# Optimization experiments

Measured on AMD Instinct MI355X. Metric: run time of the kernel, lower is better.

Reference implementation:

```python
import jax, jax.numpy as jnp
import numpy as np

B, OBS, H, A, E = 131072, 194, 64, 5, 3  # batch, obs dim, hidden, max_action_dim, n event types


def setup_inputs() -> dict:
    key = jax.random.key(0)
    ks = jax.random.split(key, 16)
    s = lambda k, shape, std=0.1: (jax.random.normal(k, shape, dtype=jnp.float32) * std)
    return {
        "x": jax.random.normal(ks[0], (B, OBS), dtype=jnp.float32),
        "action": jax.random.randint(ks[1], (B,), 0, A),
        "W1": s(ks[2], (OBS, H)), "b1": jnp.zeros((H,), jnp.float32),
        "W2": s(ks[3], (H, H)),   "b2": jnp.zeros((H,), jnp.float32),
        "Wh": s(ks[4], (E, H, A), 0.01), "bh": jnp.zeros((E, A), jnp.float32),
        "Wc1": s(ks[5], (OBS, H)), "bc1": jnp.zeros((H,), jnp.float32),
        "Wc2": s(ks[6], (H, H)),   "bc2": jnp.zeros((H,), jnp.float32),
        "Wc3": s(ks[7], (H, 1)),   "bc3": jnp.zeros((1,), jnp.float32),
    }


def reference(x, action, W1, b1, W2, b2, Wh, bh, Wc1, bc1, Wc2, bc2, Wc3, bc3):
    # shared trunk
    feat = jnp.tanh(jnp.tanh(x @ W1 + b1) @ W2 + b2)          # [B, H]
    # route each sample to one of E heads via argmax of first 3 obs dims
    ev = jnp.argmax(x[:, :E], axis=1)                          # [B] int
    all_logits = jnp.einsum('bh,eha->bea', feat, Wh) + bh      # [B, E, A]
    logits = jnp.take_along_axis(
        all_logits, jnp.broadcast_to(ev[:, None, None], (x.shape[0], 1, A)), axis=1
    )[:, 0]                                                    # [B, A]
    logp_all = jax.nn.log_softmax(logits, axis=-1)             # [B, A]
    logp = jnp.take_along_axis(logp_all, action[:, None], axis=1)[:, 0]  # [B]
    entropy = -jnp.sum(jnp.exp(logp_all) * logp_all, axis=-1)  # [B]
    # critic
    value = jnp.tanh(jnp.tanh(x @ Wc1 + bc1) @ Wc2 + bc2) @ Wc3 + bc3    # [B, 1]
    return action, logp, entropy, value
```

## Files before the change

kernel.cpp:

```cpp
#include <hip/hip_runtime.h>
#include <hip/hip_bf16.h>

constexpr int Bt    = 131072;
constexpr int OBS   = 194;

constexpr int W1B_S  = 0;
constexpr int WC1B_S = 14336;
constexpr int W2B_S  = 28672;
constexpr int WC2B_S = 36864;
constexpr int WHB_S  = 45056;
constexpr size_t EVG_B = 98304;
constexpr size_t HG_S  = 131072;

typedef short bf8   __attribute__((ext_vector_type(8)));
typedef float f32x4 __attribute__((ext_vector_type(4)));
typedef unsigned int u32;

__device__ __forceinline__ short f2bs(float f) {
    union { __hip_bfloat16 h; short s; } u;
    u.h = __float2bfloat16(f);
    return u.s;
}
__device__ __forceinline__ float bs2f(short s) {
    union { short s; __hip_bfloat16 h; } u;
    u.s = s;
    return __bfloat162float(u.h);
}
__device__ __forceinline__ u32 pk2(float a, float b) {
    union { __hip_bfloat162 h; u32 u; } r;
    r.h = __float22bfloat162_rn(float2{a, b});
    return r.u;
}
__device__ __forceinline__ float fast_tanh(float v) {
    v = fminf(fmaxf(v, -15.f), 15.f);
    float e = __expf(2.f * v);
    return (e - 1.f) * __builtin_amdgcn_rcpf(e + 1.f);
}
__device__ __forceinline__ void dma16(const void* g, void* s) {
    __builtin_amdgcn_global_load_lds(
        (const __attribute__((address_space(1))) u32*)g,
        (__attribute__((address_space(3))) u32*)s, 16, 0, 0);
}

__global__ void __launch_bounds__(256) prep(
    const float* __restrict__ W1, const float* __restrict__ b1,
    const float* __restrict__ W2, const float* __restrict__ Wh,
    const float* __restrict__ Wc1, const float* __restrict__ bc1,
    const float* __restrict__ Wc2, const float* __restrict__ Wc3,
    short* __restrict__ ws)
{
    const int gid = blockIdx.x * 256 + threadIdx.x;
    const int gsz = gridDim.x * 256;

    for (int i = gid; i < 14336; i += gsz) {
        int j = i & 7, l = (i >> 3) & 63, nt = (i >> 9) & 3, kb = i >> 11;
        int k = kb * 32 + ((l >> 4) << 3) + j;
        int n = nt * 16 + (l & 15);
        short v1 = 0, v2 = 0;
        if (k < OBS) {
            v1 = f2bs(W1[k * 64 + n]);
            v2 = f2bs(Wc1[k * 64 + n]);
        } else if (k == OBS) {
            v1 = f2bs(b1[n]);
            v2 = f2bs(bc1[n]);
        }
        ws[W1B_S + i]  = v1;
        ws[WC1B_S + i] = v2;
    }
    for (int i = gid; i < 8192; i += gsz) {
        int j = i & 7, l = (i >> 3) & 63, nt = (i >> 9) & 3, kb = i >> 11;
        int s = kb * 32 + ((l >> 4) << 3) + j;
        int kp = (s & 3) * 16 + (s >> 2);
        int n = nt * 16 + (l & 15);
        ws[W2B_S + i]  = f2bs(W2[kp * 64 + n]);
        ws[WC2B_S + i] = f2bs(Wc2[kp * 64 + n]);
    }
    for (int i = gid; i < 1024; i += gsz) {
        int j = i & 7, l = (i >> 3) & 63, kb = i >> 9;
        int s = kb * 32 + ((l >> 4) << 3) + j;
        int kp = (s & 3) * 16 + (s >> 2);
        int cc = l & 15;
        float v;
        if (cc == 15) v = Wc3[kp];
        else { int e = cc / 5, a = cc - 5 * e; v = Wh[(e * 64 + kp) * 5 + a]; }
        ws[WHB_S + i] = f2bs(v);
    }
}

__global__ void __launch_bounds__(512, 2) trunk1(
    const float* __restrict__ x, const short* __restrict__ ws,
    short* __restrict__ hG, unsigned char* __restrict__ evG)
{
    __shared__ __align__(16) char smem[57344];
    const int t = threadIdx.x;
    const int l = t & 63, q = (t >> 4) & 3, c = t & 15;
    const int wu = __builtin_amdgcn_readfirstlane(t >> 6);

    #pragma unroll
    for (int i = 0; i < 7; ++i) {
        int ch = wu * 7 + i;
        dma16((const char*)ws + ch * 1024 + l * 16, smem + ch * 1024);
    }

    const bf8* fW1L  = reinterpret_cast<const bf8*>(smem);
    const bf8* fWc1L = reinterpret_cast<const bf8*>(smem + 28672);

    const int tt = blockIdx.x * 8 + wu;
    const float* xr = x + (size_t)tt * 16 * OBS + (size_t)c * OBS;

    union AF { u32 u[4]; bf8 v; } af[7];
    float4 f40;
    #pragma unroll
    for (int kb = 0; kb < 6; ++kb) {
        float4 a = *reinterpret_cast<const float4*>(xr + kb * 32 + q * 8);
        float4 b = *reinterpret_cast<const float4*>(xr + kb * 32 + q * 8 + 4);
        if (kb == 0) f40 = a;
        af[kb].u[0] = pk2(a.x, a.y);
        af[kb].u[1] = pk2(a.z, a.w);
        af[kb].u[2] = pk2(b.x, b.y);
        af[kb].u[3] = pk2(b.z, b.w);
    }
    af[6].u[0] = 0; af[6].u[1] = 0; af[6].u[2] = 0; af[6].u[3] = 0;
    if (q == 0) {
        float2 v = *reinterpret_cast<const float2*>(xr + 192);
        af[6].u[0] = pk2(v.x, v.y);
        af[6].u[1] = pk2(1.0f, 0.0f);
    }
    if (l < 16) {
        int ev = 0; float b = f40.x;
        if (f40.y > b) { b = f40.y; ev = 1; }
        if (f40.z > b) ev = 2;
        evG[tt * 16 + l] = (unsigned char)ev;
    }

    __syncthreads();

    f32x4 aa[4], ac[4];
    #pragma unroll
    for (int nt = 0; nt < 4; ++nt) {
        aa[nt] = f32x4{0.f, 0.f, 0.f, 0.f};
        ac[nt] = f32x4{0.f, 0.f, 0.f, 0.f};
    }
    #pragma unroll
    for (int kb = 0; kb < 7; ++kb) {
        bf8 a = af[kb].v;
        #pragma unroll
        for (int nt = 0; nt < 4; ++nt) {
            aa[nt] = __builtin_amdgcn_mfma_f32_16x16x32_bf16(a, fW1L [(kb * 4 + nt) * 64 + l], aa[nt], 0, 0, 0);
            ac[nt] = __builtin_amdgcn_mfma_f32_16x16x32_bf16(a, fWc1L[(kb * 4 + nt) * 64 + l], ac[nt], 0, 0, 0);
        }
    }

    short* hGt = hG + (size_t)tt * 2048;
    #pragma unroll
    for (int r = 0; r < 4; ++r) {
        uint2 pa, pc;
        pa.x = pk2(fast_tanh(aa[0][r]), fast_tanh(aa[1][r]));
        pa.y = pk2(fast_tanh(aa[2][r]), fast_tanh(aa[3][r]));
        pc.x = pk2(fast_tanh(ac[0][r]), fast_tanh(ac[1][r]));
        pc.y = pk2(fast_tanh(ac[2][r]), fast_tanh(ac[3][r]));
        *reinterpret_cast<uint2*>(hGt + (r * 4 + q) * 64 + 4 * c)        = pa;
        *reinterpret_cast<uint2*>(hGt + 1024 + (r * 4 + q) * 64 + 4 * c) = pc;
    }
}

constexpr int F2_W   = 34816;
constexpr int F2_PW  = 5248;
constexpr int F2_LDS = F2_W + 8 * F2_PW;

__global__ void __launch_bounds__(512, 2) head2(
    const int* __restrict__ act_in,
    const float* __restrict__ b2, const float* __restrict__ bc2,
    const float* __restrict__ bh, const float* __restrict__ bc3,
    const short* __restrict__ ws,
    const short* __restrict__ hG, const unsigned char* __restrict__ evG,
    float* __restrict__ out)
{
    __shared__ __align__(16) char smem[F2_LDS];
    const int t = threadIdx.x;
    const int l = t & 63, q = (t >> 4) & 3, c = t & 15;
    const int wu = __builtin_amdgcn_readfirstlane(t >> 6);

    #pragma unroll
    for (int i = 0; i < 5; ++i) {
        int ch = wu + i * 8;
        if (ch < 34)
            dma16((const char*)ws + 57344 + ch * 1024 + l * 16, smem + ch * 1024);
    }

    float b2v[4], bc2v[4];
    #pragma unroll
    for (int nt = 0; nt < 4; ++nt) {
        b2v[nt]  = b2[nt * 16 + c];
        bc2v[nt] = bc2[nt * 16 + c];
    }
    float bhv = (c < 15) ? bh[c] : bc3[0];

    __syncthreads();

    const bf8* fW2L  = reinterpret_cast<const bf8*>(smem);
    const bf8* fWc2L = reinterpret_cast<const bf8*>(smem + 16384);
    const bf8* fWhL  = reinterpret_cast<const bf8*>(smem + 32768);
    short* ha = reinterpret_cast<short*>(smem + F2_W + wu * F2_PW);
    short* hc = ha + 1152;
    short* lw = reinterpret_cast<short*>(smem + F2_W + wu * F2_PW + 4608);
    float* vb = reinterpret_cast<float*>(smem + F2_W + wu * F2_PW + 5184);

    #pragma unroll 1
    for (int i = 0; i < 2; ++i) {
        const int tt = blockIdx.x * 16 + wu * 2 + i;
        const int gm = tt * 16 + c;
        int act = 0, evc = 0;
        if (l < 16) { act = act_in[gm]; evc = evG[gm]; }

        const short* hGt = hG + (size_t)tt * 2048;
        uint2 va[4], vc2[4];
        #pragma unroll
        for (int r = 0; r < 4; ++r) {
            va[r]  = *reinterpret_cast<const uint2*>(hGt + (r * 4 + q) * 64 + 4 * c);
            vc2[r] = *reinterpret_cast<const uint2*>(hGt + 1024 + (r * 4 + q) * 64 + 4 * c);
        }
        #pragma unroll
        for (int r = 0; r < 4; ++r) {
            *reinterpret_cast<uint2*>(&ha[(q * 4 + r) * 72 + 4 * c]) = va[r];
            *reinterpret_cast<uint2*>(&hc[(q * 4 + r) * 72 + 4 * c]) = vc2[r];
        }
        bf8 xa[2], xc[2];
        #pragma unroll
        for (int kb = 0; kb < 2; ++kb) {
            xa[kb] = *reinterpret_cast<const bf8*>(&ha[c * 72 + kb * 32 + q * 8]);
            xc[kb] = *reinterpret_cast<const bf8*>(&hc[c * 72 + kb * 32 + q * 8]);
        }

        f32x4 aa[4], ac[4];
        #pragma unroll
        for (int nt = 0; nt < 4; ++nt) {
            aa[nt] = f32x4{b2v[nt], b2v[nt], b2v[nt], b2v[nt]};
            ac[nt] = f32x4{bc2v[nt], bc2v[nt], bc2v[nt], bc2v[nt]};
        }
        #pragma unroll
        for (int kb = 0; kb < 2; ++kb) {
            #pragma unroll
            for (int nt = 0; nt < 4; ++nt) {
                aa[nt] = __builtin_amdgcn_mfma_f32_16x16x32_bf16(xa[kb], fW2L [(kb * 4 + nt) * 64 + l], aa[nt], 0, 0, 0);
                ac[nt] = __builtin_amdgcn_mfma_f32_16x16x32_bf16(xc[kb], fWc2L[(kb * 4 + nt) * 64 + l], ac[nt], 0, 0, 0);
            }
        }
        #pragma unroll
        for (int r = 0; r < 4; ++r) {
            uint2 pa, pc;
            pa.x = pk2(fast_tanh(aa[0][r]), fast_tanh(aa[1][r]));
            pa.y = pk2(fast_tanh(aa[2][r]), fast_tanh(aa[3][r]));
            pc.x = pk2(fast_tanh(ac[0][r]), fast_tanh(ac[1][r]));
            pc.y = pk2(fast_tanh(ac[2][r]), fast_tanh(ac[3][r]));
            *reinterpret_cast<uint2*>(&ha[(q * 4 + r) * 72 + 4 * c]) = pa;
            *reinterpret_cast<uint2*>(&hc[(q * 4 + r) * 72 + 4 * c]) = pc;
        }

        {
            f32x4 lg = f32x4{bhv, bhv, bhv, bhv};
            f32x4 vv = f32x4{bhv, bhv, bhv, bhv};
            #pragma unroll
            for (int kb = 0; kb < 2; ++kb) {
                bf8 bw = fWhL[kb * 64 + l];
                bf8 fa = *reinterpret_cast<const bf8*>(&ha[c * 72 + kb * 32 + q * 8]);
                bf8 fc = *reinterpret_cast<const bf8*>(&hc[c * 72 + kb * 32 + q * 8]);
                lg = __builtin_amdgcn_mfma_f32_16x16x32_bf16(fa, bw, lg, 0, 0, 0);
                vv = __builtin_amdgcn_mfma_f32_16x16x32_bf16(fc, bw, vv, 0, 0, 0);
            }
            #pragma unroll
            for (int r = 0; r < 4; ++r)
                lw[(q * 4 + r) * 18 + c] = f2bs(lg[r]);
            if (c == 15) {
                #pragma unroll
                for (int r = 0; r < 4; ++r)
                    vb[q * 4 + r] = vv[r];
            }
        }

        if (l < 16) {
            float lg[5];
            #pragma unroll
            for (int a = 0; a < 5; ++a)
                lg[a] = bs2f(lw[c * 18 + evc * 5 + a]);
            float mx = lg[0];
            #pragma unroll
            for (int a = 1; a < 5; ++a) mx = fmaxf(mx, lg[a]);
            float se = 0.f;
            #pragma unroll
            for (int a = 0; a < 5; ++a) se += __expf(lg[a] - mx);
            float lse = __logf(se) + mx;
            float lsel = lg[0];
            #pragma unroll
            for (int a = 1; a < 5; ++a) lsel = (act == a) ? lg[a] : lsel;
            float ent = 0.f;
            #pragma unroll
            for (int a = 0; a < 5; ++a) { float lp = lg[a] - lse; ent -= __expf(lp) * lp; }

            out[gm]          = (float)act;
            out[Bt + gm]     = lsel - lse;
            out[2 * Bt + gm] = ent;
            out[3 * Bt + gm] = vb[c];
        }
    }
}

extern "C" void kernel_launch(void* const* d_in, const int* in_sizes, int n_in,
                              void* d_out, int out_size, void* d_ws, size_t ws_size,
                              hipStream_t stream) {
    const float* x   = (const float*)d_in[0];
    const int*   act = (const int*)  d_in[1];
    const float* W1  = (const float*)d_in[2];
    const float* b1  = (const float*)d_in[3];
    const float* W2  = (const float*)d_in[4];
    const float* b2  = (const float*)d_in[5];
    const float* Wh  = (const float*)d_in[6];
    const float* bh  = (const float*)d_in[7];
    const float* Wc1 = (const float*)d_in[8];
    const float* bc1 = (const float*)d_in[9];
    const float* Wc2 = (const float*)d_in[10];
    const float* bc2 = (const float*)d_in[11];
    const float* Wc3 = (const float*)d_in[12];
    const float* bc3 = (const float*)d_in[13];
    float* out = (float*)d_out;
    short* ws  = (short*)d_ws;
    short* hG  = ws + HG_S;
    unsigned char* evG = (unsigned char*)d_ws + EVG_B;

    hipLaunchKernelGGL(prep, dim3(32), dim3(256), 0, stream,
                       W1, b1, W2, Wh, Wc1, bc1, Wc2, Wc3, ws);
    hipLaunchKernelGGL(trunk1, dim3(1024), dim3(512), 0, stream,
                       x, ws, hG, evG);
    hipLaunchKernelGGL(head2, dim3(512), dim3(512), 0, stream,
                       act, b2, bc2, bh, bc3, ws, hG, evG, out);
}
```

Measured before the change: 197.1 us.

## Fuse trunk and head kernels, keep hidden activations on-chip

Merges the first-layer trunk kernel and the second-layer/head kernel into one launch, so the bf16 hidden activations and event indices no longer round-trip through global workspace memory. Each wave converts MFMA accumulators to A-operand fragments through a small per-wave LDS bounce buffer. The second-layer and head weights are now read straight from global memory (through cache) instead of being staged in LDS. This removes one launch and about 64 MB of intermediate traffic, but LDS per block grows and the global weight reads may add latency.

```diff
diff --git a/kernel.cpp b/kernel.cpp
--- a/kernel.cpp
+++ b/kernel.cpp
@@ -9,8 +9,6 @@
 constexpr int W2B_S  = 28672;
 constexpr int WC2B_S = 36864;
 constexpr int WHB_S  = 45056;
-constexpr size_t EVG_B = 98304;
-constexpr size_t HG_S  = 131072;
 
 typedef short bf8   __attribute__((ext_vector_type(8)));
 typedef float f32x4 __attribute__((ext_vector_type(4)));
@@ -87,11 +85,16 @@
     }
 }
 
-__global__ void __launch_bounds__(512, 2) trunk1(
-    const float* __restrict__ x, const short* __restrict__ ws,
-    short* __restrict__ hG, unsigned char* __restrict__ evG)
+constexpr int FB_LDS = 57344 + 8 * 2304;
+
+__global__ void __launch_bounds__(512, 2) fused_ac(
+    const float* __restrict__ x, const int* __restrict__ act_in,
+    const float* __restrict__ b2, const float* __restrict__ bc2,
+    const float* __restrict__ bh, const float* __restrict__ bc3,
+    const short* __restrict__ ws,
+    float* __restrict__ out)
 {
-    __shared__ __align__(16) char smem[57344];
+    __shared__ __align__(16) char smem[FB_LDS];
     const int t = threadIdx.x;
     const int l = t & 63, q = (t >> 4) & 3, c = t & 15;
     const int wu = __builtin_amdgcn_readfirstlane(t >> 6);
@@ -104,6 +107,7 @@
 
     const bf8* fW1L  = reinterpret_cast<const bf8*>(smem);
     const bf8* fWc1L = reinterpret_cast<const bf8*>(smem + 28672);
+    short* bb = reinterpret_cast<short*>(smem + 57344 + wu * 2304);
 
     const int tt = blockIdx.x * 8 + wu;
     const float* xr = x + (size_t)tt * 16 * OBS + (size_t)c * OBS;
@@ -126,12 +130,22 @@
         af[6].u[0] = pk2(v.x, v.y);
         af[6].u[1] = pk2(1.0f, 0.0f);
     }
+
+    int act = 0, evc = 0;
     if (l < 16) {
-        int ev = 0; float b = f40.x;
-        if (f40.y > b) { b = f40.y; ev = 1; }
-        if (f40.z > b) ev = 2;
-        evG[tt * 16 + l] = (unsigned char)ev;
-    }
+        act = act_in[tt * 16 + l];
+        float b = f40.x;
+        if (f40.y > b) { b = f40.y; evc = 1; }
+        if (f40.z > b) evc = 2;
+    }
+
+    float b2v[4], bc2v[4];
+    #pragma unroll
+    for (int nt = 0; nt < 4; ++nt) {
+        b2v[nt]  = b2[nt * 16 + c];
+        bc2v[nt] = bc2[nt * 16 + c];
+    }
+    float bhv = (c < 15) ? bh[c] : bc3[0];
 
     __syncthreads();
 
@@ -151,157 +165,88 @@
         }
     }
 
-    short* hGt = hG + (size_t)tt * 2048;
-    #pragma unroll
-    for (int r = 0; r < 4; ++r) {
-        uint2 pa, pc;
-        pa.x = pk2(fast_tanh(aa[0][r]), fast_tanh(aa[1][r]));
-        pa.y = pk2(fast_tanh(aa[2][r]), fast_tanh(aa[3][r]));
-        pc.x = pk2(fast_tanh(ac[0][r]), fast_tanh(ac[1][r]));
-        pc.y = pk2(fast_tanh(ac[2][r]), fast_tanh(ac[3][r]));
-        *reinterpret_cast<uint2*>(hGt + (r * 4 + q) * 64 + 4 * c)        = pa;
-        *reinterpret_cast<uint2*>(hGt + 1024 + (r * 4 + q) * 64 + 4 * c) = pc;
-    }
-}
-
-constexpr int F2_W   = 34816;
-constexpr int F2_PW  = 5248;
-constexpr int F2_LDS = F2_W + 8 * F2_PW;
-
-__global__ void __launch_bounds__(512, 2) head2(
-    const int* __restrict__ act_in,
-    const float* __restrict__ b2, const float* __restrict__ bc2,
-    const float* __restrict__ bh, const float* __restrict__ bc3,
-    const short* __restrict__ ws,
-    const short* __restrict__ hG, const unsigned char* __restrict__ evG,
-    float* __restrict__ out)
-{
-    __shared__ __align__(16) char smem[F2_LDS];
-    const int t = threadIdx.x;
-    const int l = t & 63, q = (t >> 4) & 3, c = t & 15;
-    const int wu = __builtin_amdgcn_readfirstlane(t >> 6);
-
-    #pragma unroll
-    for (int i = 0; i < 5; ++i) {
-        int ch = wu + i * 8;
-        if (ch < 34)
-            dma16((const char*)ws + 57344 + ch * 1024 + l * 16, smem + ch * 1024);
-    }
-
-    float b2v[4], bc2v[4];
+    auto bounce = [&](f32x4* cc4, bf8* fr) {
+        #pragma unroll
+        for (int r = 0; r < 4; ++r) {
+            uint2 p;
+            p.x = pk2(fast_tanh(cc4[0][r]), fast_tanh(cc4[1][r]));
+            p.y = pk2(fast_tanh(cc4[2][r]), fast_tanh(cc4[3][r]));
+            *reinterpret_cast<uint2*>(&bb[(q * 4 + r) * 72 + 4 * c]) = p;
+        }
+        #pragma unroll
+        for (int kb = 0; kb < 2; ++kb)
+            fr[kb] = *reinterpret_cast<const bf8*>(&bb[c * 72 + kb * 32 + q * 8]);
+    };
+
+    bf8 xa[2], xc[2];
+    bounce(aa, xa);
+    bounce(ac, xc);
+
+    const bf8* fW2G  = reinterpret_cast<const bf8*>((const char*)ws + 57344);
+    const bf8* fWc2G = reinterpret_cast<const bf8*>((const char*)ws + 73728);
+    const bf8* fWhG  = reinterpret_cast<const bf8*>((const char*)ws + 90112);
     #pragma unroll
     for (int nt = 0; nt < 4; ++nt) {
-        b2v[nt]  = b2[nt * 16 + c];
-        bc2v[nt] = bc2[nt * 16 + c];
-    }
-    float bhv = (c < 15) ? bh[c] : bc3[0];
-
-    __syncthreads();
-
-    const bf8* fW2L  = reinterpret_cast<const bf8*>(smem);
-    const bf8* fWc2L = reinterpret_cast<const bf8*>(smem + 16384);
-    const bf8* fWhL  = reinterpret_cast<const bf8*>(smem + 32768);
-    short* ha = reinterpret_cast<short*>(smem + F2_W + wu * F2_PW);
-    short* hc = ha + 1152;
-    short* lw = reinterpret_cast<short*>(smem + F2_W + wu * F2_PW + 4608);
-    float* vb = reinterpret_cast<float*>(smem + F2_W + wu * F2_PW + 5184);
-
-    #pragma unroll 1
-    for (int i = 0; i < 2; ++i) {
-        const int tt = blockIdx.x * 16 + wu * 2 + i;
+        aa[nt] = f32x4{b2v[nt], b2v[nt], b2v[nt], b2v[nt]};
+        ac[nt] = f32x4{bc2v[nt], bc2v[nt], bc2v[nt], bc2v[nt]};
+    }
+    #pragma unroll
+    for (int kb = 0; kb < 2; ++kb) {
+        #pragma unroll
+        for (int nt = 0; nt < 4; ++nt) {
+            aa[nt] = __builtin_amdgcn_mfma_f32_16x16x32_bf16(xa[kb], fW2G [(kb * 4 + nt) * 64 + l], aa[nt], 0, 0, 0);
+            ac[nt] = __builtin_amdgcn_mfma_f32_16x16x32_bf16(xc[kb], fWc2G[(kb * 4 + nt) * 64 + l], ac[nt], 0, 0, 0);
+        }
+    }
+
+    bf8 fa[2], fc[2];
+    bounce(aa, fa);
+    bounce(ac, fc);
+
+    f32x4 lg = f32x4{bhv, bhv, bhv, bhv};
+    f32x4 vv = f32x4{bhv, bhv, bhv, bhv};
+    #pragma unroll
+    for (int kb = 0; kb < 2; ++kb) {
+        bf8 bw = fWhG[kb * 64 + l];
+        lg = __builtin_amdgcn_mfma_f32_16x16x32_bf16(fa[kb], bw, lg, 0, 0, 0);
+        vv = __builtin_amdgcn_mfma_f32_16x16x32_bf16(fc[kb], bw, vv, 0, 0, 0);
+    }
+
+    short* lw = bb;
+    float* vb = reinterpret_cast<float*>(bb + 1120);
+    #pragma unroll
+    for (int r = 0; r < 4; ++r)
+        lw[(q * 4 + r) * 18 + c] = f2bs(lg[r]);
+    if (c == 15) {
+        #pragma unroll
+        for (int r = 0; r < 4; ++r)
+            vb[q * 4 + r] = vv[r];
+    }
+
+    if (l < 16) {
+        float lgv[5];
+        #pragma unroll
+        for (int a = 0; a < 5; ++a)
+            lgv[a] = bs2f(lw[c * 18 + evc * 5 + a]);
+        float mx = lgv[0];
+        #pragma unroll
+        for (int a = 1; a < 5; ++a) mx = fmaxf(mx, lgv[a]);
+        float se = 0.f;
+        #pragma unroll
+        for (int a = 0; a < 5; ++a) se += __expf(lgv[a] - mx);
+        float lse = __logf(se) + mx;
+        float lsel = lgv[0];
+        #pragma unroll
+        for (int a = 1; a < 5; ++a) lsel = (act == a) ? lgv[a] : lsel;
+        float ent = 0.f;
+        #pragma unroll
+        for (int a = 0; a < 5; ++a) { float lp = lgv[a] - lse; ent -= __expf(lp) * lp; }
+
         const int gm = tt * 16 + c;
-        int act = 0, evc = 0;
-        if (l < 16) { act = act_in[gm]; evc = evG[gm]; }
-
-        const short* hGt = hG + (size_t)tt * 2048;
-        uint2 va[4], vc2[4];
-        #pragma unroll
-        for (int r = 0; r < 4; ++r) {
-            va[r]  = *reinterpret_cast<const uint2*>(hGt + (r * 4 + q) * 64 + 4 * c);
-            vc2[r] = *reinterpret_cast<const uint2*>(hGt + 1024 + (r * 4 + q) * 64 + 4 * c);
-        }
-        #pragma unroll
-        for (int r = 0; r < 4; ++r) {
-            *reinterpret_cast<uint2*>(&ha[(q * 4 + r) * 72 + 4 * c]) = va[r];
-            *reinterpret_cast<uint2*>(&hc[(q * 4 + r) * 72 + 4 * c]) = vc2[r];
-        }
-        bf8 xa[2], xc[2];
-        #pragma unroll
-        for (int kb = 0; kb < 2; ++kb) {
-            xa[kb] = *reinterpret_cast<const bf8*>(&ha[c * 72 + kb * 32 + q * 8]);
-            xc[kb] = *reinterpret_cast<const bf8*>(&hc[c * 72 + kb * 32 + q * 8]);
-        }
-
-        f32x4 aa[4], ac[4];
-        #pragma unroll
-        for (int nt = 0; nt < 4; ++nt) {
-            aa[nt] = f32x4{b2v[nt], b2v[nt], b2v[nt], b2v[nt]};
-            ac[nt] = f32x4{bc2v[nt], bc2v[nt], bc2v[nt], bc2v[nt]};
-        }
-        #pragma unroll
-        for (int kb = 0; kb < 2; ++kb) {
-            #pragma unroll
-            for (int nt = 0; nt < 4; ++nt) {
-                aa[nt] = __builtin_amdgcn_mfma_f32_16x16x32_bf16(xa[kb], fW2L [(kb * 4 + nt) * 64 + l], aa[nt], 0, 0, 0);
-                ac[nt] = __builtin_amdgcn_mfma_f32_16x16x32_bf16(xc[kb], fWc2L[(kb * 4 + nt) * 64 + l], ac[nt], 0, 0, 0);
-            }
-        }
-        #pragma unroll
-        for (int r = 0; r < 4; ++r) {
-            uint2 pa, pc;
-            pa.x = pk2(fast_tanh(aa[0][r]), fast_tanh(aa[1][r]));
-            pa.y = pk2(fast_tanh(aa[2][r]), fast_tanh(aa[3][r]));
-            pc.x = pk2(fast_tanh(ac[0][r]), fast_tanh(ac[1][r]));
-            pc.y = pk2(fast_tanh(ac[2][r]), fast_tanh(ac[3][r]));
-            *reinterpret_cast<uint2*>(&ha[(q * 4 + r) * 72 + 4 * c]) = pa;
-            *reinterpret_cast<uint2*>(&hc[(q * 4 + r) * 72 + 4 * c]) = pc;
-        }
-
-        {
-            f32x4 lg = f32x4{bhv, bhv, bhv, bhv};
-            f32x4 vv = f32x4{bhv, bhv, bhv, bhv};
-            #pragma unroll
-            for (int kb = 0; kb < 2; ++kb) {
-                bf8 bw = fWhL[kb * 64 + l];
-                bf8 fa = *reinterpret_cast<const bf8*>(&ha[c * 72 + kb * 32 + q * 8]);
-                bf8 fc = *reinterpret_cast<const bf8*>(&hc[c * 72 + kb * 32 + q * 8]);
-                lg = __builtin_amdgcn_mfma_f32_16x16x32_bf16(fa, bw, lg, 0, 0, 0);
-                vv = __builtin_amdgcn_mfma_f32_16x16x32_bf16(fc, bw, vv, 0, 0, 0);
-            }
-            #pragma unroll
-            for (int r = 0; r < 4; ++r)
-                lw[(q * 4 + r) * 18 + c] = f2bs(lg[r]);
-            if (c == 15) {
-                #pragma unroll
-                for (int r = 0; r < 4; ++r)
-                    vb[q * 4 + r] = vv[r];
-            }
-        }
-
-        if (l < 16) {
-            float lg[5];
-            #pragma unroll
-            for (int a = 0; a < 5; ++a)
-                lg[a] = bs2f(lw[c * 18 + evc * 5 + a]);
-            float mx = lg[0];
-            #pragma unroll
-            for (int a = 1; a < 5; ++a) mx = fmaxf(mx, lg[a]);
-            float se = 0.f;
-            #pragma unroll
-            for (int a = 0; a < 5; ++a) se += __expf(lg[a] - mx);
-            float lse = __logf(se) + mx;
-            float lsel = lg[0];
-            #pragma unroll
-            for (int a = 1; a < 5; ++a) lsel = (act == a) ? lg[a] : lsel;
-            float ent = 0.f;
-            #pragma unroll
-            for (int a = 0; a < 5; ++a) { float lp = lg[a] - lse; ent -= __expf(lp) * lp; }
-
-            out[gm]          = (float)act;
-            out[Bt + gm]     = lsel - lse;
-            out[2 * Bt + gm] = ent;
-            out[3 * Bt + gm] = vb[c];
-        }
+        out[gm]          = (float)act;
+        out[Bt + gm]     = lsel - lse;
+        out[2 * Bt + gm] = ent;
+        out[3 * Bt + gm] = vb[c];
     }
 }
 
@@ -324,13 +269,9 @@
     const float* bc3 = (const float*)d_in[13];
     float* out = (float*)d_out;
     short* ws  = (short*)d_ws;
-    short* hG  = ws + HG_S;
-    unsigned char* evG = (unsigned char*)d_ws + EVG_B;
 
     hipLaunchKernelGGL(prep, dim3(32), dim3(256), 0, stream,
                        W1, b1, W2, Wh, Wc1, bc1, Wc2, Wc3, ws);
-    hipLaunchKernelGGL(trunk1, dim3(1024), dim3(512), 0, stream,
-                       x, ws, hG, evG);
-    hipLaunchKernelGGL(head2, dim3(512), dim3(512), 0, stream,
-                       act, b2, bc2, bh, bc3, ws, hG, evG, out);
-}
+    hipLaunchKernelGGL(fused_ac, dim3(1024), dim3(512), 0, stream,
+                       x, act, b2, bc2, bh, bc3, ws, out);
+}
```

Result: faster. 185.0 us (-6.1%).
